# Performance work log

Measured on AMD Instinct MI355X. Metric: run time of the kernel, lower is better.

The kernel has to match this reference:

```python
import jax, jax.numpy as jnp
import numpy as np
import math

B, T, DIM = 2, 2048, 4096
N_HEADS, N_KV_HEADS = 32, 8
HEAD_DIM = DIM // N_HEADS          # 128
N_REP = N_HEADS // N_KV_HEADS      # 4
ROPE_THETA = 500000.0
NEG_INF = -1e9


def setup_inputs() -> dict:
    key = jax.random.key(0)
    ks = jax.random.split(key, 5)
    x = jax.random.normal(ks[0], (B, T, DIM), dtype=jnp.float32)
    # rotary angles: theta_j = pos * base^(-2j/d), shape [T, HEAD_DIM//2]
    inv_freq = 1.0 / (ROPE_THETA ** (jnp.arange(0, HEAD_DIM, 2, dtype=jnp.float32) / HEAD_DIM))
    freqs = jnp.arange(T, dtype=jnp.float32)[:, None] * inv_freq[None, :]
    # causal additive mask [T, T]
    mask = jnp.where(jnp.tril(jnp.ones((T, T), dtype=bool)), 0.0, NEG_INF).astype(jnp.float32)
    s = 0.02
    wq = jax.random.normal(ks[1], (DIM, N_HEADS * HEAD_DIM), dtype=jnp.float32) * s
    wk = jax.random.normal(ks[2], (DIM, N_KV_HEADS * HEAD_DIM), dtype=jnp.float32) * s
    wv = jax.random.normal(ks[3], (DIM, N_KV_HEADS * HEAD_DIM), dtype=jnp.float32) * s
    wo = jax.random.normal(ks[4], (N_HEADS * HEAD_DIM, DIM), dtype=jnp.float32) * s
    return {"x": x, "freqs": freqs, "mask": mask, "wq": wq, "wk": wk, "wv": wv, "wo": wo, "start_pos": 0}


def _apply_rope(x, cos, sin):
    # x: [B, T, H, D]; cos/sin: [T, D//2]; adjacent pairs rotated (view-as-complex)
    xr = x[..., 0::2]
    xi = x[..., 1::2]
    c = cos[None, :, None, :]
    s = sin[None, :, None, :]
    out_r = xr * c - xi * s
    out_i = xr * s + xi * c
    return jnp.stack([out_r, out_i], axis=-1).reshape(x.shape)


def reference(x, freqs, mask, wq, wk, wv, wo, start_pos):
    Bx, Tx, C = x.shape
    xq = (x @ wq).reshape(Bx, Tx, N_HEADS, HEAD_DIM)
    xk = (x @ wk).reshape(Bx, Tx, N_KV_HEADS, HEAD_DIM)
    xv = (x @ wv).reshape(Bx, Tx, N_KV_HEADS, HEAD_DIM)
    cos, sin = jnp.cos(freqs), jnp.sin(freqs)
    xq = _apply_rope(xq, cos, sin)
    xk = _apply_rope(xk, cos, sin)
    # repeat_kv for GQA: [B, T, Hkv, D] -> [B, T, Hkv*n_rep, D]
    xk = jnp.repeat(xk, N_REP, axis=2)
    xv = jnp.repeat(xv, N_REP, axis=2)
    q = xq.transpose(0, 2, 1, 3)  # [B, H, T, D]
    k = xk.transpose(0, 2, 1, 3)
    v = xv.transpose(0, 2, 1, 3)
    scores = jnp.einsum("bhtd,bhsd->bhts", q, k) / math.sqrt(HEAD_DIM)
    scores = scores + mask[None, None, :, :]
    probs = jax.nn.softmax(scores.astype(jnp.float32), axis=-1).astype(q.dtype)
    out = jnp.einsum("bhts,bhsd->bhtd", probs, v)
    out = out.transpose(0, 2, 1, 3).reshape(Bx, Tx, -1)
    return out @ wo
```

## Files before the change

### kernel.cpp

```cpp
#include <hip/hip_runtime.h>
#include <cstdint>
#include <cstddef>

typedef float  f32x4  __attribute__((ext_vector_type(4)));
typedef short  bf16x8 __attribute__((ext_vector_type(8)));
typedef unsigned short u16;
typedef u16    u16x8  __attribute__((ext_vector_type(8)));
typedef unsigned int u32;

#define T_SEQ 2048
#define N_HEADS 32
#define N_KVH 8
#define HD 128

__device__ __forceinline__ u16 f2bf(float f){
  union { float f; unsigned u; } v; v.f = f;
  unsigned u = v.u;
  u += 0x7fffu + ((u >> 16) & 1u);
  return (u16)(u >> 16);
}

__device__ __forceinline__ u32 cvt_pk_bf16(float a, float b){
  u32 r;
  asm volatile("v_cvt_pk_bf16_f32 %0, %1, %2" : "=v"(r) : "v"(a), "v"(b));
  return r;
}

__device__ __forceinline__ void gll16(const void* g, void* l){
  __builtin_amdgcn_global_load_lds((const __attribute__((address_space(1))) void*)g,
                                   (__attribute__((address_space(3))) void*)l, 16, 0, 0);
}

__global__ void mk_tables(const float* __restrict__ f, float* __restrict__ c, float* __restrict__ s){
  int i = blockIdx.x*256 + threadIdx.x;
  float v = f[i];
  c[i] = cosf(v);
  s[i] = sinf(v);
}

__global__ void cvt_bf16(const float* __restrict__ in, u16* __restrict__ out){
  size_t i = (size_t)blockIdx.x*256 + threadIdx.x;
  const float4* p = (const float4*)(in + i*8);
  float4 a = p[0], b = p[1];
  u16x8 o;
  o[0]=f2bf(a.x); o[1]=f2bf(a.y); o[2]=f2bf(a.z); o[3]=f2bf(a.w);
  o[4]=f2bf(b.x); o[5]=f2bf(b.y); o[6]=f2bf(b.z); o[7]=f2bf(b.w);
  *(u16x8*)(out + i*8) = o;
}

__global__ void wtrans(const float* __restrict__ W, u16* __restrict__ Wt, int K, int N){
  __shared__ float t[32][33];
  int tx = threadIdx.x, ty = threadIdx.y;
  int nb = blockIdx.x*32, kb = blockIdx.y*32;
#pragma unroll
  for (int j=0;j<4;j++) t[ty+8*j][tx] = W[(size_t)(kb+ty+8*j)*N + nb + tx];
  __syncthreads();
#pragma unroll
  for (int j=0;j<4;j++) Wt[(size_t)(nb+ty+8*j)*K + kb + tx] = f2bf(t[tx][ty+8*j]);
}

template<int BN>
__global__ __launch_bounds__(512, 2) void gemm256(
    const u16* __restrict__ A, const u16* __restrict__ Bt,
    float* __restrict__ C, int N, int K)
{
  constexpr int NGB = BN/64;
  constexpr int NF  = BN/64;
  __shared__ u16 Ab[2][16384];
  __shared__ u16 Bb[2][BN*64];
  const int tid = threadIdx.x;
  const int w = tid >> 6, lane = tid & 63;
  const int lo = lane & 15, hi = lane >> 4;

  const int nbx = N / BN;
  const int cpx = (int)gridDim.x >> 3;
  const int swzb = ((int)blockIdx.x & 7)*cpx + ((int)blockIdx.x >> 3);
  const int bx = swzb % nbx, by = swzb / nbx;
  const int m0 = by << 8, n0 = bx * BN;
  const int wm = w >> 2, wn = w & 3;

  const int rA = tid >> 3;
  const int chg = (tid & 7) ^ (rA & 7);
  const size_t srcoff = (size_t)rA * K + chg*8;
  const u16* Ag = A  + (size_t)m0*K + srcoff;
  const u16* Bg = Bt + (size_t)n0*K + srcoff;
  const int dstc = (w*64)*8;

  f32x4 acc[8][NF];
#pragma unroll
  for (int i=0;i<8;i++)
#pragma unroll
    for (int j=0;j<NF;j++) acc[i][j] = (f32x4){0.f,0.f,0.f,0.f};

  const int NT = K >> 6;
#pragma unroll
  for (int j=0;j<4;j++)   gll16(Ag + (size_t)j*64*K, &Ab[0][j*4096 + dstc]);
#pragma unroll
  for (int j=0;j<NGB;j++) gll16(Bg + (size_t)j*64*K, &Bb[0][j*4096 + dstc]);

  const int sw = lo & 7;
#pragma unroll 1
  for (int t=0; t<NT; ++t){
    const int cur = t & 1;
    if (t > 0){
      asm volatile("s_waitcnt lgkmcnt(0)" ::: "memory");
      __builtin_amdgcn_s_barrier();
    }
    if (t + 1 < NT){
      const int kt = (t+1) << 6;
      const int nxt = cur ^ 1;
#pragma unroll
      for (int j=0;j<4;j++)   gll16(Ag + (size_t)j*64*K + kt, &Ab[nxt][j*4096 + dstc]);
#pragma unroll
      for (int j=0;j<NGB;j++) gll16(Bg + (size_t)j*64*K + kt, &Bb[nxt][j*4096 + dstc]);
      if constexpr (BN == 256){
        asm volatile("s_waitcnt vmcnt(8)" ::: "memory");
      } else {
        asm volatile("s_waitcnt vmcnt(6)" ::: "memory");
      }
    } else {
      asm volatile("s_waitcnt vmcnt(0)" ::: "memory");
    }
    __builtin_amdgcn_s_barrier();
    __builtin_amdgcn_sched_barrier(0);

    const u16* Ac = &Ab[cur][0] + (wm*128)*64;
    const u16* Bc = &Bb[cur][0] + (wn*(BN/4))*64;
    bf16x8 a[4], b[NF];
#pragma unroll
    for (int ks=0; ks<2; ks++){
      const int ch = ((ks*4 + hi) ^ sw) << 3;
#pragma unroll
      for (int g=0; g<NF; g++) b[g] = *(const bf16x8*)(Bc + (g*16 + lo)*64 + ch);
#pragma unroll
      for (int mh=0; mh<2; mh++){
#pragma unroll
        for (int f=0; f<4; f++) a[f] = *(const bf16x8*)(Ac + (mh*64 + f*16 + lo)*64 + ch);
        __builtin_amdgcn_s_setprio(1);
#pragma unroll
        for (int f=0; f<4; f++)
#pragma unroll
          for (int g=0; g<NF; g++)
            acc[mh*4+f][g] = __builtin_amdgcn_mfma_f32_16x16x32_bf16(a[f], b[g], acc[mh*4+f][g], 0, 0, 0);
        __builtin_amdgcn_s_setprio(0);
      }
    }
  }

#pragma unroll
  for (int mh=0; mh<2; mh++)
#pragma unroll
    for (int f=0; f<4; f++)
#pragma unroll
      for (int g=0; g<NF; g++)
#pragma unroll
        for (int r=0; r<4; r++)
          C[(size_t)(m0 + wm*128 + mh*64 + f*16 + hi*4 + r)*N + n0 + wn*(BN/4) + g*16 + lo] = acc[mh*4+f][g][r];
}

__global__ void rope_q(const float* __restrict__ qf, const float* __restrict__ c,
                       const float* __restrict__ s, u16* __restrict__ qb){
  const int row = blockIdx.x;
  const int t = row & (T_SEQ-1);
  const float* ib = qf + (size_t)row*4096;
  u16* ob = qb + (size_t)row*4096;
#pragma unroll
  for (int k=0;k<8;k++){
    int p = threadIdx.x + k*256;
    int i = p & 63;
    float cv = c[t*64+i], sv = s[t*64+i];
    float2 v = *(const float2*)(ib + 2*p);
    float vr = v.x*cv - v.y*sv;
    float vi = v.x*sv + v.y*cv;
    ushort2 o; o.x = f2bf(vr*0.12751743648963412f); o.y = f2bf(vi*0.12751743648963412f);
    *(ushort2*)(ob + 2*p) = o;
  }
}

__global__ void rope_k(const float* __restrict__ kvf, const float* __restrict__ c,
                       const float* __restrict__ s, u16* __restrict__ kb){
  const int row = blockIdx.x;
  const int b = row >> 11, t = row & (T_SEQ-1);
  const float* ib = kvf + (size_t)row*2048;
#pragma unroll
  for (int k=0;k<2;k++){
    int p = threadIdx.x + k*256;
    int kvh = p >> 6, i = p & 63;
    float cv = c[t*64+i], sv = s[t*64+i];
    float2 v = *(const float2*)(ib + 2*p);
    float vr = v.x*cv - v.y*sv;
    float vi = v.x*sv + v.y*cv;
    u16* o = kb + ((size_t)(b*N_KVH+kvh)*T_SEQ + t)*HD + 2*i;
    ushort2 ov; ov.x = f2bf(vr); ov.y = f2bf(vi);
    *(ushort2*)o = ov;
  }
}

__global__ void vtrans(const float* __restrict__ kvf, u16* __restrict__ vt){
  __shared__ float tl[32][33];
  int tx = threadIdx.x, ty = threadIdx.y;
  int t0 = blockIdx.x*32, d0 = blockIdx.y*32, bh = blockIdx.z;
  int b = bh >> 3, kvh = bh & 7;
#pragma unroll
  for (int j=0;j<4;j++)
    tl[ty+8*j][tx] = kvf[(size_t)(b*T_SEQ + t0+ty+8*j)*2048 + 1024 + kvh*HD + d0 + tx];
  __syncthreads();
#pragma unroll
  for (int j=0;j<4;j++)
    vt[((size_t)bh*HD + d0+ty+8*j)*T_SEQ + t0 + tx] = f2bf(tl[tx][ty+8*j]);
}

#define KVB 64
__global__ __launch_bounds__(512) void attn_kernel(
    const u16* __restrict__ qb, const u16* __restrict__ kb,
    const u16* __restrict__ vt, u16* __restrict__ attn)
{
  __shared__ u16 KV[2][2][8192];

  const int tid = threadIdx.x;
  const int lane = tid & 63, wid = tid >> 6;
  const int lo = lane & 15, hi = lane >> 4;
  const bool lowhi = (hi < 2);
  const int bp0 = lo + 32*(hi & 1);
  const int bp1 = bp0 + 16;
  const int pairI = blockIdx.x;
  const int h = blockIdx.y, b = blockIdx.z;
  const int kvh = h >> 2;

  int koff[2], voff[2];
#pragma unroll
  for (int p=0;p<2;p++){
    int s = p*512 + tid;
    int kr = s >> 4, kch = (s & 15) ^ (kr & 7);
    koff[p] = kr*HD + kch*8;
    int vd = s >> 3, vch = (s & 7) ^ (vd & 7);
    voff[p] = vd*T_SEQ + vch*8;
  }
  const u16* Kg = kb + (size_t)(b*N_KVH + kvh)*T_SEQ*HD;
  const u16* Vg = vt + (size_t)(b*N_KVH + kvh)*HD*T_SEQ;

#pragma unroll 1
  for (int pass=0; pass<2; ++pass){
    const int qt = pass ? pairI : (7 - pairI);
    const int q0 = qt*256 + wid*32;
    const int ntiles = (qt+1)*4;

    bf16x8 qfr[2][4];
#pragma unroll
    for (int mb=0;mb<2;mb++){
      const u16* qrow = qb + (size_t)(b*T_SEQ + q0 + mb*16 + lo)*4096 + h*HD;
#pragma unroll
      for (int kc=0;kc<4;kc++) qfr[mb][kc] = *(const bf16x8*)(qrow + kc*32 + hi*8);
    }

    f32x4 acc[2][8];
#pragma unroll
    for (int mb=0;mb<2;mb++)
#pragma unroll
      for (int nd=0;nd<8;nd++) acc[mb][nd] = (f32x4){0.f,0.f,0.f,0.f};
    float m_[2] = {-3.0e38f, -3.0e38f};
    float l_[2] = {0.f, 0.f};

    if (pass){
      asm volatile("s_waitcnt lgkmcnt(0)" ::: "memory");
      __builtin_amdgcn_s_barrier();
    }
#pragma unroll
    for (int p=0;p<2;p++){
      gll16(Kg + koff[p], (u16*)&KV[0][0][0] + (p*512 + wid*64)*8);
      gll16(Vg + voff[p], (u16*)&KV[0][1][0] + (p*512 + wid*64)*8);
    }

#pragma unroll 1
    for (int st=0; st<ntiles; ++st){
      const int cur = st & 1;
      const int sb = st*KVB;
      if (st > 0){
        asm volatile("s_waitcnt lgkmcnt(0)" ::: "memory");
        __builtin_amdgcn_s_barrier();
      }
      if (st + 1 < ntiles){
        const int nxt = cur ^ 1;
        const int nb2 = (st+1)*KVB;
#pragma unroll
        for (int p=0;p<2;p++){
          gll16(Kg + nb2*HD + koff[p], (u16*)&KV[nxt][0][0] + (p*512 + wid*64)*8);
          gll16(Vg + nb2    + voff[p], (u16*)&KV[nxt][1][0] + (p*512 + wid*64)*8);
        }
        asm volatile("s_waitcnt vmcnt(4)" ::: "memory");
      } else {
        asm volatile("s_waitcnt vmcnt(0)" ::: "memory");
      }
      __builtin_amdgcn_s_barrier();

      const bool live = (sb <= q0 + 31);
      if (live){
        f32x4 sc[2][4];
#pragma unroll
        for (int mb=0;mb<2;mb++)
#pragma unroll
          for (int ns=0;ns<4;ns++) sc[mb][ns] = (f32x4){0.f,0.f,0.f,0.f};
        __builtin_amdgcn_s_setprio(1);
#pragma unroll
        for (int ns=0;ns<4;ns++){
          const int row = ns*16 + lo;
          const u16* klp = (const u16*)&KV[cur][0][0] + row*HD;
          const int sw = row & 7;
          bf16x8 kf[4];
#pragma unroll
          for (int kc=0;kc<4;kc++) kf[kc] = *(const bf16x8*)(klp + (((kc*4+hi)^sw)<<3));
#pragma unroll
          for (int kc=0;kc<4;kc++){
            sc[0][ns] = __builtin_amdgcn_mfma_f32_16x16x32_bf16(kf[kc], qfr[0][kc], sc[0][ns], 0, 0, 0);
            sc[1][ns] = __builtin_amdgcn_mfma_f32_16x16x32_bf16(kf[kc], qfr[1][kc], sc[1][ns], 0, 0, 0);
          }
        }
        __builtin_amdgcn_s_setprio(0);

        if (sb + 63 > q0){
#pragma unroll
          for (int mb=0;mb<2;mb++){
            const int qg = q0 + mb*16 + lo;
#pragma unroll
            for (int ns=0;ns<4;ns++)
#pragma unroll
              for (int r=0;r<4;r++){
                int sg = sb + ns*16 + hi*4 + r;
                if (sg > qg) sc[mb][ns][r] = -3.0e38f;
              }
          }
        }

        bf16x8 pa[2][2];
#pragma unroll
        for (int mb=0;mb<2;mb++){
          float mx = fmaxf(fmaxf(fmaxf(sc[mb][0][0],sc[mb][0][1]),fmaxf(sc[mb][0][2],sc[mb][0][3])),
                     fmaxf(fmaxf(fmaxf(sc[mb][1][0],sc[mb][1][1]),fmaxf(sc[mb][1][2],sc[mb][1][3])),
                           fmaxf(fmaxf(sc[mb][2][0],sc[mb][2][1]),
                                 fmaxf(fmaxf(sc[mb][2][2],sc[mb][2][3]),
                                       fmaxf(fmaxf(sc[mb][3][0],sc[mb][3][1]),fmaxf(sc[mb][3][2],sc[mb][3][3]))))));
          mx = fmaxf(mx, __shfl_xor(mx, 16));
          mx = fmaxf(mx, __shfl_xor(mx, 32));
          if (__any(mx > m_[mb] + 8.f)){
            float mn = fmaxf(m_[mb], mx);
            float scal = exp2f(m_[mb] - mn);
            m_[mb] = mn;
            l_[mb] *= scal;
            float srow[4];
#pragma unroll
            for (int r=0;r<4;r++) srow[r] = __shfl(scal, hi*4+r);
#pragma unroll
            for (int nd=0;nd<8;nd++)
#pragma unroll
              for (int r=0;r<4;r++) acc[mb][nd][r] *= srow[r];
          }
          float rs = 0.f;
#pragma unroll
          for (int ns=0;ns<4;ns++)
#pragma unroll
            for (int r=0;r<4;r++){
              sc[mb][ns][r] = exp2f(sc[mb][ns][r] - m_[mb]);
              rs += sc[mb][ns][r];
            }
          rs += __shfl_xor(rs, 16);
          rs += __shfl_xor(rs, 32);
          l_[mb] += rs;

#pragma unroll
          for (int k2=0;k2<2;k2++){
            u32 P0 = cvt_pk_bf16(sc[mb][2*k2][0],   sc[mb][2*k2][1]);
            u32 P1 = cvt_pk_bf16(sc[mb][2*k2][2],   sc[mb][2*k2][3]);
            u32 Q0 = cvt_pk_bf16(sc[mb][2*k2+1][0], sc[mb][2*k2+1][1]);
            u32 Q1 = cvt_pk_bf16(sc[mb][2*k2+1][2], sc[mb][2*k2+1][3]);
            u32 pA0 = (u32)__shfl((int)P0, bp0);
            u32 pA1 = (u32)__shfl((int)P1, bp0);
            u32 pA2 = (u32)__shfl((int)P0, bp1);
            u32 pA3 = (u32)__shfl((int)P1, bp1);
            u32 qA0 = (u32)__shfl((int)Q0, bp0);
            u32 qA1 = (u32)__shfl((int)Q1, bp0);
            u32 qA2 = (u32)__shfl((int)Q0, bp1);
            u32 qA3 = (u32)__shfl((int)Q1, bp1);
            union { u32 w[4]; bf16x8 v; } pk;
            pk.w[0] = lowhi ? pA0 : qA0;
            pk.w[1] = lowhi ? pA1 : qA1;
            pk.w[2] = lowhi ? pA2 : qA2;
            pk.w[3] = lowhi ? pA3 : qA3;
            pa[mb][k2] = pk.v;
          }
        }

        __builtin_amdgcn_s_setprio(1);
#pragma unroll
        for (int nd=0;nd<8;nd++){
          const int d = nd*16 + lo;
          const u16* vlp = (const u16*)&KV[cur][1][0] + d*64;
          const int sw = d & 7;
          bf16x8 vf[2];
#pragma unroll
          for (int k2=0;k2<2;k2++) vf[k2] = *(const bf16x8*)(vlp + (((k2*4+hi)^sw)<<3));
#pragma unroll
          for (int k2=0;k2<2;k2++){
            acc[0][nd] = __builtin_amdgcn_mfma_f32_16x16x32_bf16(pa[0][k2], vf[k2], acc[0][nd], 0, 0, 0);
            acc[1][nd] = __builtin_amdgcn_mfma_f32_16x16x32_bf16(pa[1][k2], vf[k2], acc[1][nd], 0, 0, 0);
          }
        }
        __builtin_amdgcn_s_setprio(0);
      }
    }

#pragma unroll
    for (int mb=0;mb<2;mb++){
      float inv = 1.f / l_[mb];
      float invr[4];
#pragma unroll
      for (int r=0;r<4;r++) invr[r] = __shfl(inv, hi*4+r);
      u16* ob = attn + (size_t)(b*T_SEQ + q0 + mb*16 + hi*4)*4096 + h*HD;
#pragma unroll
      for (int nd=0;nd<8;nd++)
#pragma unroll
        for (int r=0;r<4;r++)
          ob[(size_t)r*4096 + nd*16 + lo] = f2bf(acc[mb][nd][r]*invr[r]);
    }
  }
}

extern "C" void kernel_launch(void* const* d_in, const int* in_sizes, int n_in,
                              void* d_out, int out_size, void* d_ws, size_t ws_size,
                              hipStream_t stream)
{
  (void)in_sizes; (void)n_in; (void)out_size; (void)ws_size;
  const float* x     = (const float*)d_in[0];
  const float* freqs = (const float*)d_in[1];
  const float* wq    = (const float*)d_in[3];
  const float* wk    = (const float*)d_in[4];
  const float* wv    = (const float*)d_in[5];
  const float* wo    = (const float*)d_in[6];

  char* ws = (char*)d_ws;
  float* cost = (float*)(ws + 0);
  float* sint = (float*)(ws + 524288);
  u16* xb   = (u16*)(ws + 1048576);
  u16* wqt  = (u16*)(ws + 34603008);
  u16* wkt  = (u16*)(ws + 68157440);
  u16* wvt  = (u16*)(ws + 76546048);
  u16* qbuf = (u16*)(ws + 84934656);
  u16* kbuf = (u16*)(ws + 118489088);
  u16* vbuf = (u16*)(ws + 126877696);
  u16* attnb = xb;
  u16* wot   = wqt;

  float* qf  = (float*)d_out;
  float* kvf = (float*)d_out;

  dim3 tb(32, 8);

  mk_tables<<<512, 256, 0, stream>>>(freqs, cost, sint);
  cvt_bf16<<<8192, 256, 0, stream>>>(x, xb);
  wtrans<<<dim3(128,128), tb, 0, stream>>>(wq, wqt, 4096, 4096);
  wtrans<<<dim3(32,128),  tb, 0, stream>>>(wk, wkt, 4096, 1024);
  wtrans<<<dim3(32,128),  tb, 0, stream>>>(wv, wvt, 4096, 1024);

  gemm256<256><<<dim3(256), 512, 0, stream>>>(xb, wqt, qf, 4096, 4096);
  rope_q<<<4096, 256, 0, stream>>>(qf, cost, sint, qbuf);

  gemm256<128><<<dim3(256), 512, 0, stream>>>(xb, wkt, kvf, 2048, 4096);
  rope_k<<<4096, 256, 0, stream>>>(kvf, cost, sint, kbuf);
  vtrans<<<dim3(64,4,16), tb, 0, stream>>>(kvf, vbuf);

  attn_kernel<<<dim3(4,32,2), 512, 0, stream>>>(qbuf, kbuf, vbuf, attnb);

  wtrans<<<dim3(128,128), tb, 0, stream>>>(wo, wot, 4096, 4096);
  gemm256<256><<<dim3(256), 512, 0, stream>>>(attnb, wot, (float*)d_out, 4096, 4096);
}
```

Measured before the change: 576.4 us.

## Add 4-stage pipelined 8-phase GEMM kernel for Q and output projections

Adds a new bf16 MFMA GEMM kernel that keeps four K-slices in shared memory and interleaves global-to-LDS loads with eight MFMA phases per two iterations. Each phase is separated by barriers and raised wave priority. The Q projection and the output projection now use it in place of gemm256<256>. The aim is to hide global memory latency behind MFMA work. In exchange it uses 128 KB of LDS per block, more barriers, and a hand-written prologue and epilogue that must match the tile count exactly.

```diff
diff --git a/kernel.cpp b/kernel.cpp
--- a/kernel.cpp
+++ b/kernel.cpp
@@ -156,6 +156,146 @@
 #pragma unroll
         for (int r=0; r<4; r++)
           C[(size_t)(m0 + wm*128 + mh*64 + f*16 + hi*4 + r)*N + n0 + wn*(BN/4) + g*16 + lo] = acc[mh*4+f][g][r];
+}
+
+#define DSA8(MH, RG) { _Pragma("unroll") for (int f=0; f<4; f++) a[f] = *(const bf16x8*)(AL + (RG) + La[MH][f]); }
+#define DSB8(RG)     { _Pragma("unroll") for (int g=0; g<4; g++) b[g] = *(const bf16x8*)(BL + (RG) + Lb[g]); }
+#define STGA8(RG, KO) { gll16(Ag + offs0 + (KO), AL + (RG) + wofs); gll16(Ag + offs1 + (KO), AL + (RG) + 4096 + wofs); }
+#define STGB8(RG, KO) { gll16(Bg + offs0 + (KO), BL + (RG) + wofs); gll16(Bg + offs1 + (KO), BL + (RG) + 4096 + wofs); }
+#define MFMA16(MH) { _Pragma("unroll") for (int f=0; f<4; f++) _Pragma("unroll") for (int g=0; g<4; g++) \
+    acc[(MH)*4+f][g] = __builtin_amdgcn_mfma_f32_16x16x32_bf16(a[f], b[g], acc[(MH)*4+f][g], 0, 0, 0); }
+#define PH_SYNC() { __builtin_amdgcn_sched_barrier(0); __builtin_amdgcn_s_barrier(); \
+    asm volatile("s_waitcnt lgkmcnt(0)" ::: "memory"); __builtin_amdgcn_sched_barrier(0); }
+#define PH_END() { __builtin_amdgcn_s_setprio(0); __builtin_amdgcn_s_barrier(); }
+
+__global__ __launch_bounds__(512, 2) void gemm8p(
+    const u16* __restrict__ A, const u16* __restrict__ Bt,
+    float* __restrict__ C, int N, int K)
+{
+  __shared__ u16 AL[32768];
+  __shared__ u16 BL[32768];
+  const int tid = threadIdx.x;
+  const int w = tid >> 6, lane = tid & 63;
+  const int lo = lane & 15, hi = lane >> 4;
+
+  const int nbx = N >> 8;
+  const int cpx = (int)gridDim.x >> 3;
+  const int swzb = ((int)blockIdx.x & 7)*cpx + ((int)blockIdx.x >> 3);
+  const int bx = swzb % nbx, by = swzb / nbx;
+  const int m0 = by << 8, n0 = bx << 8;
+  const int wm = w >> 2, wn = w & 3;
+
+  int La[2][4], Lb[4];
+#pragma unroll
+  for (int mh=0; mh<2; mh++)
+#pragma unroll
+    for (int f=0; f<4; f++){
+      int row = wm*128 + mh*64 + f*16 + lo;
+      int p = row >> 1;
+      La[mh][f] = (p*8 + ((hi*2 + (row&1)) ^ (p&7)))*8;
+    }
+#pragma unroll
+  for (int g=0; g<4; g++){
+    int row = wn*64 + g*16 + lo;
+    int p = row >> 1;
+    Lb[g] = (p*8 + ((hi*2 + (row&1)) ^ (p&7)))*8;
+  }
+
+  int offs0, offs1;
+  {
+    int n = tid;
+    int p = n>>3, cb = (n&7) ^ (p&7);
+    offs0 = (p*2 + (cb&1))*K + (cb>>1)*8;
+    n = 512 + tid;
+    p = n>>3; cb = (n&7) ^ (p&7);
+    offs1 = (p*2 + (cb&1))*K + (cb>>1)*8;
+  }
+  const u16* Ag = A  + (size_t)m0*K;
+  const u16* Bg = Bt + (size_t)n0*K;
+  const int wofs = w*512;
+
+  f32x4 acc[8][4];
+#pragma unroll
+  for (int i=0;i<8;i++)
+#pragma unroll
+    for (int j=0;j<4;j++) acc[i][j] = (f32x4){0.f,0.f,0.f,0.f};
+
+  const int NT = K >> 6;
+  bf16x8 a[4], b[4];
+
+  STGA8(0, 0)       STGB8(0, 0)
+  STGA8(8192, 32)   STGB8(8192, 32)
+  STGA8(16384, 64)  STGB8(16384, 64)
+  asm volatile("s_waitcnt vmcnt(8)" ::: "memory");
+  __builtin_amdgcn_s_barrier();
+
+#pragma unroll 1
+  for (int u = 0; u < NT-2; u += 2){
+    const int ku = u*64;
+    DSA8(0, 0) DSB8(0)
+    STGA8(24576, ku+96)
+    PH_SYNC() __builtin_amdgcn_s_setprio(1); MFMA16(0) PH_END()
+    DSA8(1, 0)
+    STGB8(24576, ku+96)
+    asm volatile("s_waitcnt vmcnt(8)" ::: "memory");
+    PH_SYNC() __builtin_amdgcn_s_setprio(1); MFMA16(1) PH_END()
+    DSA8(0, 8192) DSB8(8192)
+    STGA8(0, ku+128)
+    PH_SYNC() __builtin_amdgcn_s_setprio(1); MFMA16(0) PH_END()
+    DSA8(1, 8192)
+    STGB8(0, ku+128)
+    asm volatile("s_waitcnt vmcnt(8)" ::: "memory");
+    PH_SYNC() __builtin_amdgcn_s_setprio(1); MFMA16(1) PH_END()
+    DSA8(0, 16384) DSB8(16384)
+    STGA8(8192, ku+160)
+    PH_SYNC() __builtin_amdgcn_s_setprio(1); MFMA16(0) PH_END()
+    DSA8(1, 16384)
+    STGB8(8192, ku+160)
+    asm volatile("s_waitcnt vmcnt(8)" ::: "memory");
+    PH_SYNC() __builtin_amdgcn_s_setprio(1); MFMA16(1) PH_END()
+    DSA8(0, 24576) DSB8(24576)
+    STGA8(16384, ku+192)
+    PH_SYNC() __builtin_amdgcn_s_setprio(1); MFMA16(0) PH_END()
+    DSA8(1, 24576)
+    STGB8(16384, ku+192)
+    asm volatile("s_waitcnt vmcnt(8)" ::: "memory");
+    PH_SYNC() __builtin_amdgcn_s_setprio(1); MFMA16(1) PH_END()
+  }
+
+  {
+    const int ku = (NT-2)*64;
+    DSA8(0, 0) DSB8(0)
+    STGA8(24576, ku+96)
+    PH_SYNC() __builtin_amdgcn_s_setprio(1); MFMA16(0) PH_END()
+    DSA8(1, 0)
+    STGB8(24576, ku+96)
+    asm volatile("s_waitcnt vmcnt(8)" ::: "memory");
+    PH_SYNC() __builtin_amdgcn_s_setprio(1); MFMA16(1) PH_END()
+    DSA8(0, 8192) DSB8(8192)
+    PH_SYNC() __builtin_amdgcn_s_setprio(1); MFMA16(0) PH_END()
+    DSA8(1, 8192)
+    asm volatile("s_waitcnt vmcnt(4)" ::: "memory");
+    PH_SYNC() __builtin_amdgcn_s_setprio(1); MFMA16(1) PH_END()
+    DSA8(0, 16384) DSB8(16384)
+    PH_SYNC() __builtin_amdgcn_s_setprio(1); MFMA16(0) PH_END()
+    DSA8(1, 16384)
+    asm volatile("s_waitcnt vmcnt(0)" ::: "memory");
+    PH_SYNC() __builtin_amdgcn_s_setprio(1); MFMA16(1) PH_END()
+    DSA8(0, 24576) DSB8(24576)
+    PH_SYNC() __builtin_amdgcn_s_setprio(1); MFMA16(0) PH_END()
+    DSA8(1, 24576)
+    PH_SYNC() __builtin_amdgcn_s_setprio(1); MFMA16(1) PH_END()
+  }
+
+#pragma unroll
+  for (int mh=0; mh<2; mh++)
+#pragma unroll
+    for (int f=0; f<4; f++)
+#pragma unroll
+      for (int g=0; g<4; g++)
+#pragma unroll
+        for (int r=0; r<4; r++)
+          C[(size_t)(m0 + wm*128 + mh*64 + f*16 + hi*4 + r)*N + n0 + wn*64 + g*16 + lo] = acc[mh*4+f][g][r];
 }
 
 __global__ void rope_q(const float* __restrict__ qf, const float* __restrict__ c,
@@ -460,7 +600,7 @@
   wtrans<<<dim3(32,128),  tb, 0, stream>>>(wk, wkt, 4096, 1024);
   wtrans<<<dim3(32,128),  tb, 0, stream>>>(wv, wvt, 4096, 1024);
 
-  gemm256<256><<<dim3(256), 512, 0, stream>>>(xb, wqt, qf, 4096, 4096);
+  gemm8p<<<dim3(256), 512, 0, stream>>>(xb, wqt, qf, 4096, 4096);
   rope_q<<<4096, 256, 0, stream>>>(qf, cost, sint, qbuf);
 
   gemm256<128><<<dim3(256), 512, 0, stream>>>(xb, wkt, kvf, 2048, 4096);
@@ -470,5 +610,5 @@
   attn_kernel<<<dim3(4,32,2), 512, 0, stream>>>(qbuf, kbuf, vbuf, attnb);
 
   wtrans<<<dim3(128,128), tb, 0, stream>>>(wo, wot, 4096, 4096);
-  gemm256<256><<<dim3(256), 512, 0, stream>>>(attnb, wot, (float*)d_out, 4096, 4096);
-}
+  gemm8p<<<dim3(256), 512, 0, stream>>>(attnb, wot, (float*)d_out, 4096, 4096);
+}
```

After: 575.2 us. No clear change (-0.2%).
